# Kernel tuning notes

Hardware: AMD Instinct MI355X
Metric: run time of the kernel (lower is better)

## Reference

```python
import jax, jax.numpy as jnp
import numpy as np

V, B, F = 4, 8192, 128  # views, batch, fea_out
EPS = 1e-5  # torch BatchNorm1d default eps


def setup_inputs() -> dict:
    key = jax.random.key(0)
    k1, k2 = jax.random.split(key)
    x = jax.random.normal(k1, (V, B, F), dtype=jnp.float32)
    # Linear(F*F -> F) weight/bias; scale ~ kaiming-ish to keep activations sane
    W = jax.random.normal(k2, (F, F * F), dtype=jnp.float32) * 0.01
    b = jnp.zeros((F,), dtype=jnp.float32)
    gamma = jnp.ones((F,), dtype=jnp.float32)   # BN weight
    beta = jnp.zeros((F,), dtype=jnp.float32)   # BN bias
    return {"x": x, "W": W, "b": b, "gamma": gamma, "beta": beta}


def reference(x, W, b, gamma, beta):
    # x: [V, B, F] stack of views. Original loops over pairs (i<j):
    #   outer = x[i][:, :, None] @ x[j][:, None, :]          -> [B, F, F]
    #   flat  = outer.view(B, F*F)   (flat index = i*F + j)
    #   out   = ReLU(BN(Linear(flat)))
    # We fuse: Linear(flat(outer)) == einsum over W reshaped to [F_out, F, F],
    # avoiding the [B, F*F] intermediate. Same math.
    Vn, Bn, Fn = x.shape
    ii, jj = np.triu_indices(Vn, k=1)          # P = V*(V-1)/2 pairs
    x1 = x[ii]                                  # [P, B, F]
    x2 = x[jj]                                  # [P, B, F]
    Wr = W.reshape(Fn, Fn, Fn)                  # [F_out, F_i, F_j], matches row-major flatten
    # bilinear form per pair/batch: y[p,b,o] = sum_ij x1[p,b,i] * Wr[o,i,j] * x2[p,b,j] + b[o]
    y = jnp.einsum('pbi,oij,pbj->pbo', x1, Wr, x2) + b
    # BatchNorm1d in training mode: per-call batch stats (over batch axis, per pair),
    # biased variance, then affine, then ReLU.
    mean = jnp.mean(y, axis=1, keepdims=True)
    var = jnp.var(y, axis=1, keepdims=True)
    y_hat = (y - mean) * jax.lax.rsqrt(var + EPS)
    out = jax.nn.relu(gamma * y_hat + beta)     # [P, B, F]
    return out
```

## Files before the change

kernel.cpp:

```cpp
#include <hip/hip_runtime.h>

#define Fdim 128
#define Bsz  8192
#define Pn   6
#define EPSI 1e-5f
#define X2P 136
#define X1P 72

typedef _Float16 half8  __attribute__((ext_vector_type(8)));
typedef _Float16 half4t __attribute__((ext_vector_type(4)));
typedef float    float4t __attribute__((ext_vector_type(4)));

__constant__ int PAIR_A[6] = {0,0,0,1,1,2};
__constant__ int PAIR_B[6] = {1,2,3,2,3,3};

__global__ __launch_bounds__(256) void wprep(const float* __restrict__ W,
                                             _Float16* __restrict__ Wws) {
    int t    = blockIdx.x * 256 + threadIdx.x;
    int c    = t >> 9;
    int r    = t & 511;
    int nt   = r >> 6;
    int lane = r & 63;
    int q    = lane >> 4;
    int ol   = lane & 15;
    int o    = nt * 16 + ol;
    const float4t* src = (const float4t*)(W + (size_t)o * 16384 + c * 32 + q * 8);
    float4t a0 = src[0];
    float4t a1 = src[1];
    half8 h;
    h[0] = (_Float16)a0[0]; h[1] = (_Float16)a0[1];
    h[2] = (_Float16)a0[2]; h[3] = (_Float16)a0[3];
    h[4] = (_Float16)a1[0]; h[5] = (_Float16)a1[1];
    h[6] = (_Float16)a1[2]; h[7] = (_Float16)a1[3];
    *(half8*)(Wws + (size_t)t * 8) = h;
}

__global__ __launch_bounds__(256, 3) void gemm(const float* __restrict__ x,
                                               const _Float16* __restrict__ Wws,
                                               _Float16* __restrict__ yws,
                                               float* __restrict__ ssum,
                                               float* __restrict__ ssq) {
    __shared__ _Float16 x2t[128 * X2P];
    __shared__ _Float16 x1th[128 * X1P];

    int bid  = blockIdx.x;
    int p    = bid >> 7;
    int rem  = bid & 127;
    int mblk = rem >> 1;
    int nh   = rem & 1;
    int m0   = mblk * 128;
    int v1   = PAIR_A[p];
    int v2   = PAIR_B[p];
    int tid  = threadIdx.x;

    {
        const float4t* s2p = (const float4t*)(x + ((size_t)v2 * Bsz + m0) * Fdim);
        for (int it = 0; it < 16; ++it) {
            int idx = it * 256 + tid;
            int row = idx >> 5;
            int col = (idx & 31) * 4;
            float4t b = s2p[idx];
            half4t h2; h2[0]=(_Float16)b[0]; h2[1]=(_Float16)b[1];
                       h2[2]=(_Float16)b[2]; h2[3]=(_Float16)b[3];
            *(half4t*)&x2t[row * X2P + col] = h2;
        }
    }

    int lane  = tid & 63;
    int w     = tid >> 6;
    int wrow  = w >> 1;
    int wcol  = w & 1;
    int ol    = lane & 15;
    int q     = lane >> 4;
    int ntg0  = nh * 4 + wcol * 2;
    int ntg1  = ntg0 + 1;
    int rbase = wrow * 64;

    float4t acc[4][2];
#pragma unroll
    for (int mt = 0; mt < 4; ++mt) {
        acc[mt][0] = (float4t){0.f, 0.f, 0.f, 0.f};
        acc[mt][1] = (float4t){0.f, 0.f, 0.f, 0.f};
    }

    const half8* wb = (const half8*)Wws;
    const size_t woff0 = (size_t)ntg0 * 64 + lane;
    const size_t woff1 = (size_t)ntg1 * 64 + lane;
    const float* x1src = x + ((size_t)v1 * Bsz + m0) * Fdim;

    for (int kh = 0; kh < 2; ++kh) {
        if (kh) __syncthreads();
        for (int it = 0; it < 8; ++it) {
            int idx = it * 256 + tid;
            int row = idx >> 4;
            int c4  = (idx & 15) * 4;
            float4t a = *(const float4t*)(x1src + (size_t)row * Fdim + kh * 64 + c4);
            half4t h1; h1[0]=(_Float16)a[0]; h1[1]=(_Float16)a[1];
                       h1[2]=(_Float16)a[2]; h1[3]=(_Float16)a[3];
            *(half4t*)&x1th[row * X1P + c4] = h1;
        }
        __syncthreads();

        int ibase = kh * 64;
        for (int jc = 0; jc < 4; ++jc) {
            half8 x2f[4];
#pragma unroll
            for (int mt = 0; mt < 4; ++mt)
                x2f[mt] = *(const half8*)&x2t[(rbase + mt * 16 + ol) * X2P + jc * 32 + q * 8];

            half8 bfa0 = wb[(size_t)((ibase + 0) * 4 + jc) * 512 + woff0];
            half8 bfa1 = wb[(size_t)((ibase + 0) * 4 + jc) * 512 + woff1];
            half8 bfb0 = wb[(size_t)((ibase + 1) * 4 + jc) * 512 + woff0];
            half8 bfb1 = wb[(size_t)((ibase + 1) * 4 + jc) * 512 + woff1];

            for (int i8 = 0; i8 < 8; ++i8) {
                half8 x1f[4];
#pragma unroll
                for (int mt = 0; mt < 4; ++mt)
                    x1f[mt] = *(const half8*)&x1th[(rbase + mt * 16 + ol) * X1P + i8 * 8];
#pragma unroll
                for (int ii = 0; ii < 8; ++ii) {
                    int il  = i8 * 8 + ii;
                    int ipl = (il < 62) ? (il + 2) : 63;
                    half8 bn0 = wb[(size_t)((ibase + ipl) * 4 + jc) * 512 + woff0];
                    half8 bn1 = wb[(size_t)((ibase + ipl) * 4 + jc) * 512 + woff1];
#pragma unroll
                    for (int mt = 0; mt < 4; ++mt) {
                        _Float16 sc = x1f[mt][ii];
                        half8 a = x2f[mt] * sc;
                        acc[mt][0] = __builtin_amdgcn_mfma_f32_16x16x32_f16(a, bfa0, acc[mt][0], 0, 0, 0);
                        acc[mt][1] = __builtin_amdgcn_mfma_f32_16x16x32_f16(a, bfa1, acc[mt][1], 0, 0, 0);
                    }
                    bfa0 = bfb0; bfa1 = bfb1;
                    bfb0 = bn0;  bfb1 = bn1;
                }
            }
        }
    }

    float sum0 = 0.f, sq0 = 0.f, sum1 = 0.f, sq1 = 0.f;
    int col0 = ntg0 * 16 + ol;
    int col1 = ntg1 * 16 + ol;
#pragma unroll
    for (int mt = 0; mt < 4; ++mt) {
#pragma unroll
        for (int r = 0; r < 4; ++r) {
            size_t row = (size_t)p * Bsz + m0 + rbase + mt * 16 + q * 4 + r;
            float v0 = acc[mt][0][r];
            sum0 += v0; sq0 += v0 * v0;
            yws[row * Fdim + col0] = (_Float16)v0;
            float v1e = acc[mt][1][r];
            sum1 += v1e; sq1 += v1e * v1e;
            yws[row * Fdim + col1] = (_Float16)v1e;
        }
    }
    sum0 += __shfl_xor(sum0, 16, 64);  sum0 += __shfl_xor(sum0, 32, 64);
    sq0  += __shfl_xor(sq0, 16, 64);   sq0  += __shfl_xor(sq0, 32, 64);
    sum1 += __shfl_xor(sum1, 16, 64);  sum1 += __shfl_xor(sum1, 32, 64);
    sq1  += __shfl_xor(sq1, 16, 64);   sq1  += __shfl_xor(sq1, 32, 64);
    if (q == 0) {
        atomicAdd(&ssum[p * Fdim + col0], sum0);
        atomicAdd(&ssq [p * Fdim + col0], sq0);
        atomicAdd(&ssum[p * Fdim + col1], sum1);
        atomicAdd(&ssq [p * Fdim + col1], sq1);
    }
}

__global__ __launch_bounds__(256) void bnrelu(const _Float16* __restrict__ yws,
                                              const float* __restrict__ ssum,
                                              const float* __restrict__ ssq,
                                              const float* __restrict__ gamma,
                                              const float* __restrict__ beta,
                                              float* __restrict__ out) {
    __shared__ float gs[128], sh[128];
    size_t ebase = (size_t)blockIdx.x * 1024;
    int p = (int)(ebase >> 20);
    int t = threadIdx.x;
    if (t < 128) {
        float mean = ssum[p * Fdim + t] * (1.0f / 8192.0f);
        float var  = ssq [p * Fdim + t] * (1.0f / 8192.0f) - mean * mean;
        float g    = gamma[t] * rsqrtf(var + EPSI);
        gs[t] = g;
        sh[t] = beta[t] - g * mean;
    }
    __syncthreads();
    size_t e0 = ebase + (size_t)t * 4;
    int o0 = (int)(e0 & 127);
    half4t y = *(const half4t*)(yws + e0);
    float4t r;
#pragma unroll
    for (int l = 0; l < 4; ++l) {
        float v = fmaf(gs[o0 + l], (float)y[l], sh[o0 + l]);
        r[l] = v > 0.f ? v : 0.f;
    }
    *(float4t*)(out + e0) = r;
}

extern "C" void kernel_launch(void* const* d_in, const int* in_sizes, int n_in,
                              void* d_out, int out_size, void* d_ws, size_t ws_size,
                              hipStream_t stream) {
    const float* x     = (const float*)d_in[0];
    const float* W     = (const float*)d_in[1];
    const float* gamma = (const float*)d_in[3];
    const float* beta  = (const float*)d_in[4];
    float* out = (float*)d_out;

    char* ws = (char*)d_ws;
    _Float16* yws = (_Float16*)ws;
    _Float16* Wws = (_Float16*)(ws + 12582912);
    float*    ssum = (float*)(ws + 16777216);
    float*    ssq  = ssum + Pn * Fdim;

    (void)hipMemsetAsync(ssum, 0, 2 * Pn * Fdim * sizeof(float), stream);
    wprep<<<1024, 256, 0, stream>>>(W, Wws);
    gemm<<<768, 256, 0, stream>>>(x, Wws, yws, ssum, ssq);
    bnrelu<<<6144, 256, 0, stream>>>(yws, ssum, ssq, gamma, beta, out);
}
```

Measured before the change: 268.9 us.

## Split K across wave pairs so each wave computes four N tiles

Reassigns warps so the two waves in each row pair split the j-chunk (K) dimension instead of the output columns. Each wave now accumulates a 64x64 output tile (four N tiles) over half of K. The point is to reuse each scaled x2 A-fragment across four MFMAs instead of two, which halves the per-MFMA A-scaling work. In exchange, partial sums must be reduced through shared memory at the end, which adds barriers, and each wave holds twice as many accumulator registers. That extra register pressure may hurt occupancy under launch_bounds(256,3).

New measurement: 814.2 us. 203% more time.

```diff
diff --git a/kernel.cpp b/kernel.cpp
--- a/kernel.cpp
+++ b/kernel.cpp
@@ -40,8 +40,8 @@
                                                _Float16* __restrict__ yws,
                                                float* __restrict__ ssum,
                                                float* __restrict__ ssq) {
-    __shared__ _Float16 x2t[128 * X2P];
-    __shared__ _Float16 x1th[128 * X1P];
+    __shared__ __align__(16) _Float16 x2t[128 * X2P];
+    __shared__ __align__(16) _Float16 x1th[128 * X1P];
 
     int bid  = blockIdx.x;
     int p    = bid >> 7;
@@ -69,23 +69,20 @@
     int lane  = tid & 63;
     int w     = tid >> 6;
     int wrow  = w >> 1;
-    int wcol  = w & 1;
+    int kw    = w & 1;
     int ol    = lane & 15;
     int q     = lane >> 4;
-    int ntg0  = nh * 4 + wcol * 2;
-    int ntg1  = ntg0 + 1;
     int rbase = wrow * 64;
 
-    float4t acc[4][2];
-#pragma unroll
-    for (int mt = 0; mt < 4; ++mt) {
-        acc[mt][0] = (float4t){0.f, 0.f, 0.f, 0.f};
-        acc[mt][1] = (float4t){0.f, 0.f, 0.f, 0.f};
-    }
+    float4t acc[4][4];
+#pragma unroll
+    for (int mt = 0; mt < 4; ++mt)
+#pragma unroll
+        for (int nt = 0; nt < 4; ++nt)
+            acc[mt][nt] = (float4t){0.f, 0.f, 0.f, 0.f};
 
     const half8* wb = (const half8*)Wws;
-    const size_t woff0 = (size_t)ntg0 * 64 + lane;
-    const size_t woff1 = (size_t)ntg1 * 64 + lane;
+    const size_t wlane = (size_t)nh * 256 + lane;
     const float* x1src = x + ((size_t)v1 * Bsz + m0) * Fdim;
 
     for (int kh = 0; kh < 2; ++kh) {
@@ -101,68 +98,92 @@
         }
         __syncthreads();
 
-        int ibase = kh * 64;
-        for (int jc = 0; jc < 4; ++jc) {
+        for (int jcl = 0; jcl < 2; ++jcl) {
+            int jc = kw * 2 + jcl;
             half8 x2f[4];
 #pragma unroll
             for (int mt = 0; mt < 4; ++mt)
                 x2f[mt] = *(const half8*)&x2t[(rbase + mt * 16 + ol) * X2P + jc * 32 + q * 8];
 
-            half8 bfa0 = wb[(size_t)((ibase + 0) * 4 + jc) * 512 + woff0];
-            half8 bfa1 = wb[(size_t)((ibase + 0) * 4 + jc) * 512 + woff1];
-            half8 bfb0 = wb[(size_t)((ibase + 1) * 4 + jc) * 512 + woff0];
-            half8 bfb1 = wb[(size_t)((ibase + 1) * 4 + jc) * 512 + woff1];
-
-            for (int i8 = 0; i8 < 8; ++i8) {
+            size_t wbase = (size_t)(kh * 256 + jc) * 512 + wlane;
+            half8 bfa[4], bfb[4];
+#pragma unroll
+            for (int nt = 0; nt < 4; ++nt) bfa[nt] = wb[wbase + nt * 64];
+#pragma unroll
+            for (int nt = 0; nt < 4; ++nt) bfb[nt] = wb[wbase + 2048 + nt * 64];
+
+            for (int il8 = 0; il8 < 8; ++il8) {
                 half8 x1f[4];
 #pragma unroll
                 for (int mt = 0; mt < 4; ++mt)
-                    x1f[mt] = *(const half8*)&x1th[(rbase + mt * 16 + ol) * X1P + i8 * 8];
+                    x1f[mt] = *(const half8*)&x1th[(rbase + mt * 16 + ol) * X1P + il8 * 8];
 #pragma unroll
                 for (int ii = 0; ii < 8; ++ii) {
-                    int il  = i8 * 8 + ii;
+                    int il  = il8 * 8 + ii;
                     int ipl = (il < 62) ? (il + 2) : 63;
-                    half8 bn0 = wb[(size_t)((ibase + ipl) * 4 + jc) * 512 + woff0];
-                    half8 bn1 = wb[(size_t)((ibase + ipl) * 4 + jc) * 512 + woff1];
+                    half8 bn[4];
+#pragma unroll
+                    for (int nt = 0; nt < 4; ++nt)
+                        bn[nt] = wb[wbase + (size_t)ipl * 2048 + nt * 64];
 #pragma unroll
                     for (int mt = 0; mt < 4; ++mt) {
                         _Float16 sc = x1f[mt][ii];
                         half8 a = x2f[mt] * sc;
-                        acc[mt][0] = __builtin_amdgcn_mfma_f32_16x16x32_f16(a, bfa0, acc[mt][0], 0, 0, 0);
-                        acc[mt][1] = __builtin_amdgcn_mfma_f32_16x16x32_f16(a, bfa1, acc[mt][1], 0, 0, 0);
+#pragma unroll
+                        for (int nt = 0; nt < 4; ++nt)
+                            acc[mt][nt] = __builtin_amdgcn_mfma_f32_16x16x32_f16(a, bfa[nt], acc[mt][nt], 0, 0, 0);
                     }
-                    bfa0 = bfb0; bfa1 = bfb1;
-                    bfb0 = bn0;  bfb1 = bn1;
+#pragma unroll
+                    for (int nt = 0; nt < 4; ++nt) { bfa[nt] = bfb[nt]; bfb[nt] = bn[nt]; }
                 }
             }
         }
     }
 
-    float sum0 = 0.f, sq0 = 0.f, sum1 = 0.f, sq1 = 0.f;
-    int col0 = ntg0 * 16 + ol;
-    int col1 = ntg1 * 16 + ol;
-#pragma unroll
-    for (int mt = 0; mt < 4; ++mt) {
-#pragma unroll
-        for (int r = 0; r < 4; ++r) {
-            size_t row = (size_t)p * Bsz + m0 + rbase + mt * 16 + q * 4 + r;
-            float v0 = acc[mt][0][r];
-            sum0 += v0; sq0 += v0 * v0;
-            yws[row * Fdim + col0] = (_Float16)v0;
-            float v1e = acc[mt][1][r];
-            sum1 += v1e; sq1 += v1e * v1e;
-            yws[row * Fdim + col1] = (_Float16)v1e;
-        }
-    }
-    sum0 += __shfl_xor(sum0, 16, 64);  sum0 += __shfl_xor(sum0, 32, 64);
-    sq0  += __shfl_xor(sq0, 16, 64);   sq0  += __shfl_xor(sq0, 32, 64);
-    sum1 += __shfl_xor(sum1, 16, 64);  sum1 += __shfl_xor(sum1, 32, 64);
-    sq1  += __shfl_xor(sq1, 16, 64);   sq1  += __shfl_xor(sq1, 32, 64);
-    if (q == 0) {
-        atomicAdd(&ssum[p * Fdim + col0], sum0);
-        atomicAdd(&ssq [p * Fdim + col0], sq0);
-        atomicAdd(&ssum[p * Fdim + col1], sum1);
-        atomicAdd(&ssq [p * Fdim + col1], sq1);
+    __syncthreads();
+    float4t* xch = (float4t*)x2t;
+    if (kw == 1) {
+#pragma unroll
+        for (int mt = 0; mt < 4; ++mt)
+#pragma unroll
+            for (int nt = 0; nt < 4; ++nt)
+                xch[wrow * 1024 + (mt * 4 + nt) * 64 + lane] = acc[mt][nt];
+    }
+    __syncthreads();
+    if (kw == 0) {
+#pragma unroll
+        for (int mt = 0; mt < 4; ++mt)
+#pragma unroll
+            for (int nt = 0; nt < 4; ++nt)
+                acc[mt][nt] += xch[wrow * 1024 + (mt * 4 + nt) * 64 + lane];
+
+        float sum[4] = {0.f, 0.f, 0.f, 0.f};
+        float sq[4]  = {0.f, 0.f, 0.f, 0.f};
+#pragma unroll
+        for (int mt = 0; mt < 4; ++mt) {
+#pragma unroll
+            for (int r = 0; r < 4; ++r) {
+                size_t row = (size_t)p * Bsz + m0 + rbase + mt * 16 + q * 4 + r;
+#pragma unroll
+                for (int nt = 0; nt < 4; ++nt) {
+                    float v = acc[mt][nt][r];
+                    sum[nt] += v; sq[nt] += v * v;
+                    yws[row * Fdim + nh * 64 + nt * 16 + ol] = (_Float16)v;
+                }
+            }
+        }
+#pragma unroll
+        for (int nt = 0; nt < 4; ++nt) {
+            sum[nt] += __shfl_xor(sum[nt], 16, 64);  sum[nt] += __shfl_xor(sum[nt], 32, 64);
+            sq[nt]  += __shfl_xor(sq[nt], 16, 64);   sq[nt]  += __shfl_xor(sq[nt], 32, 64);
+        }
+        if (q == 0) {
+#pragma unroll
+            for (int nt = 0; nt < 4; ++nt) {
+                atomicAdd(&ssum[p * Fdim + nh * 64 + nt * 16 + ol], sum[nt]);
+                atomicAdd(&ssq [p * Fdim + nh * 64 + nt * 16 + ol], sq[nt]);
+            }
+        }
     }
 }
 
```

## Switch bilinear GEMM to 32x32x16 MFMA with relaid W and ring prefetch

Applied to the files above, without the earlier changes.

The main GEMM moves from 16x16x32 to 32x32x16 MFMA tiles. Each wave now covers a 64x32 output tile with two 16-wide accumulators, which halves the per-step scaling multiplies of the x2 fragments and the number of MFMA issues. W is preprocessed into a matching 32-column fragment layout and streamed through a four-deep register ring, with sched barriers added to steer the compiler's scheduling. LDS padding is reduced to 130 and 66 halves, which leaves 16-byte fragment reads on non-16-byte-aligned addresses and may cause split or slower LDS accesses.

Result: slower. 287.7 us (+7.0%).

```diff
diff --git a/kernel.cpp b/kernel.cpp
--- a/kernel.cpp
+++ b/kernel.cpp
@@ -4,12 +4,13 @@
 #define Bsz  8192
 #define Pn   6
 #define EPSI 1e-5f
-#define X2P 136
-#define X1P 72
-
-typedef _Float16 half8  __attribute__((ext_vector_type(8)));
-typedef _Float16 half4t __attribute__((ext_vector_type(4)));
+#define X2P 130
+#define X1P 66
+
+typedef _Float16 half8   __attribute__((ext_vector_type(8)));
+typedef _Float16 half4t  __attribute__((ext_vector_type(4)));
 typedef float    float4t __attribute__((ext_vector_type(4)));
+typedef float    float16t __attribute__((ext_vector_type(16)));
 
 __constant__ int PAIR_A[6] = {0,0,0,1,1,2};
 __constant__ int PAIR_B[6] = {1,2,3,2,3,3};
@@ -17,14 +18,16 @@
 __global__ __launch_bounds__(256) void wprep(const float* __restrict__ W,
                                              _Float16* __restrict__ Wws) {
     int t    = blockIdx.x * 256 + threadIdx.x;
-    int c    = t >> 9;
-    int r    = t & 511;
-    int nt   = r >> 6;
-    int lane = r & 63;
-    int q    = lane >> 4;
-    int ol   = lane & 15;
-    int o    = nt * 16 + ol;
-    const float4t* src = (const float4t*)(W + (size_t)o * 16384 + c * 32 + q * 8);
+    int f    = t >> 6;
+    int lane = t & 63;
+    int ntile = f >> 10;
+    int jc    = (f >> 7) & 7;
+    int i     = f & 127;
+    int q1 = lane >> 5;
+    int nn = lane & 31;
+    int n  = ntile * 32 + nn;
+    int k0 = i * 128 + jc * 16 + q1 * 8;
+    const float4t* src = (const float4t*)(W + (size_t)n * 16384 + k0);
     float4t a0 = src[0];
     float4t a1 = src[1];
     half8 h;
@@ -40,8 +43,8 @@
                                                _Float16* __restrict__ yws,
                                                float* __restrict__ ssum,
                                                float* __restrict__ ssq) {
-    __shared__ _Float16 x2t[128 * X2P];
-    __shared__ _Float16 x1th[128 * X1P];
+    __shared__ __align__(16) _Float16 x2t[128 * X2P];
+    __shared__ __align__(16) _Float16 x1th[128 * X1P];
 
     int bid  = blockIdx.x;
     int p    = bid >> 7;
@@ -70,22 +73,19 @@
     int w     = tid >> 6;
     int wrow  = w >> 1;
     int wcol  = w & 1;
-    int ol    = lane & 15;
-    int q     = lane >> 4;
-    int ntg0  = nh * 4 + wcol * 2;
-    int ntg1  = ntg0 + 1;
+    int nn    = lane & 31;
+    int q1    = lane >> 5;
+    int ntile = nh * 2 + wcol;
     int rbase = wrow * 64;
 
-    float4t acc[4][2];
-#pragma unroll
-    for (int mt = 0; mt < 4; ++mt) {
-        acc[mt][0] = (float4t){0.f, 0.f, 0.f, 0.f};
-        acc[mt][1] = (float4t){0.f, 0.f, 0.f, 0.f};
-    }
+    float16t acc[2];
+#pragma unroll
+    for (int mt = 0; mt < 2; ++mt)
+#pragma unroll
+        for (int e = 0; e < 16; ++e)
+            acc[mt][e] = 0.f;
 
     const half8* wb = (const half8*)Wws;
-    const size_t woff0 = (size_t)ntg0 * 64 + lane;
-    const size_t woff1 = (size_t)ntg1 * 64 + lane;
     const float* x1src = x + ((size_t)v1 * Bsz + m0) * Fdim;
 
     for (int kh = 0; kh < 2; ++kh) {
@@ -101,68 +101,56 @@
         }
         __syncthreads();
 
-        int ibase = kh * 64;
-        for (int jc = 0; jc < 4; ++jc) {
-            half8 x2f[4];
-#pragma unroll
-            for (int mt = 0; mt < 4; ++mt)
-                x2f[mt] = *(const half8*)&x2t[(rbase + mt * 16 + ol) * X2P + jc * 32 + q * 8];
-
-            half8 bfa0 = wb[(size_t)((ibase + 0) * 4 + jc) * 512 + woff0];
-            half8 bfa1 = wb[(size_t)((ibase + 0) * 4 + jc) * 512 + woff1];
-            half8 bfb0 = wb[(size_t)((ibase + 1) * 4 + jc) * 512 + woff0];
-            half8 bfb1 = wb[(size_t)((ibase + 1) * 4 + jc) * 512 + woff1];
-
-            for (int i8 = 0; i8 < 8; ++i8) {
-                half8 x1f[4];
-#pragma unroll
-                for (int mt = 0; mt < 4; ++mt)
-                    x1f[mt] = *(const half8*)&x1th[(rbase + mt * 16 + ol) * X1P + i8 * 8];
+#pragma unroll 1
+        for (int jc = 0; jc < 8; ++jc) {
+            half8 x2f[2];
+#pragma unroll
+            for (int mt = 0; mt < 2; ++mt)
+                x2f[mt] = *(const half8*)&x2t[(rbase + mt * 32 + nn) * X2P + jc * 16 + q1 * 8];
+
+            unsigned woff = (unsigned)((ntile * 1024 + jc * 128 + kh * 64) * 64 + lane);
+            half8 wbuf[4];
+#pragma unroll
+            for (int d = 0; d < 4; ++d) wbuf[d] = wb[woff + d * 64];
+
+#pragma unroll
+            for (int il8 = 0; il8 < 8; ++il8) {
+                half8 x1f[2];
+#pragma unroll
+                for (int mt = 0; mt < 2; ++mt)
+                    x1f[mt] = *(const half8*)&x1th[(rbase + mt * 32 + nn) * X1P + il8 * 8];
 #pragma unroll
                 for (int ii = 0; ii < 8; ++ii) {
-                    int il  = i8 * 8 + ii;
-                    int ipl = (il < 62) ? (il + 2) : 63;
-                    half8 bn0 = wb[(size_t)((ibase + ipl) * 4 + jc) * 512 + woff0];
-                    half8 bn1 = wb[(size_t)((ibase + ipl) * 4 + jc) * 512 + woff1];
-#pragma unroll
-                    for (int mt = 0; mt < 4; ++mt) {
-                        _Float16 sc = x1f[mt][ii];
-                        half8 a = x2f[mt] * sc;
-                        acc[mt][0] = __builtin_amdgcn_mfma_f32_16x16x32_f16(a, bfa0, acc[mt][0], 0, 0, 0);
-                        acc[mt][1] = __builtin_amdgcn_mfma_f32_16x16x32_f16(a, bfa1, acc[mt][1], 0, 0, 0);
-                    }
-                    bfa0 = bfb0; bfa1 = bfb1;
-                    bfb0 = bn0;  bfb1 = bn1;
+                    const int il = il8 * 8 + ii;
+                    half8 a0 = x2f[0] * x1f[0][ii];
+                    half8 a1 = x2f[1] * x1f[1][ii];
+                    acc[0] = __builtin_amdgcn_mfma_f32_32x32x16_f16(a0, wbuf[il & 3], acc[0], 0, 0, 0);
+                    acc[1] = __builtin_amdgcn_mfma_f32_32x32x16_f16(a1, wbuf[il & 3], acc[1], 0, 0, 0);
+                    wbuf[il & 3] = wb[woff + (unsigned)(il + 4) * 64];
                 }
+                __builtin_amdgcn_sched_barrier(0);
             }
         }
     }
 
-    float sum0 = 0.f, sq0 = 0.f, sum1 = 0.f, sq1 = 0.f;
-    int col0 = ntg0 * 16 + ol;
-    int col1 = ntg1 * 16 + ol;
-#pragma unroll
-    for (int mt = 0; mt < 4; ++mt) {
-#pragma unroll
-        for (int r = 0; r < 4; ++r) {
-            size_t row = (size_t)p * Bsz + m0 + rbase + mt * 16 + q * 4 + r;
-            float v0 = acc[mt][0][r];
-            sum0 += v0; sq0 += v0 * v0;
-            yws[row * Fdim + col0] = (_Float16)v0;
-            float v1e = acc[mt][1][r];
-            sum1 += v1e; sq1 += v1e * v1e;
-            yws[row * Fdim + col1] = (_Float16)v1e;
-        }
-    }
-    sum0 += __shfl_xor(sum0, 16, 64);  sum0 += __shfl_xor(sum0, 32, 64);
-    sq0  += __shfl_xor(sq0, 16, 64);   sq0  += __shfl_xor(sq0, 32, 64);
-    sum1 += __shfl_xor(sum1, 16, 64);  sum1 += __shfl_xor(sum1, 32, 64);
-    sq1  += __shfl_xor(sq1, 16, 64);   sq1  += __shfl_xor(sq1, 32, 64);
-    if (q == 0) {
-        atomicAdd(&ssum[p * Fdim + col0], sum0);
-        atomicAdd(&ssq [p * Fdim + col0], sq0);
-        atomicAdd(&ssum[p * Fdim + col1], sum1);
-        atomicAdd(&ssq [p * Fdim + col1], sq1);
+    float sum = 0.f, sq = 0.f;
+    int colg = ntile * 32 + nn;
+#pragma unroll
+    for (int mt = 0; mt < 2; ++mt) {
+#pragma unroll
+        for (int r = 0; r < 16; ++r) {
+            int rl = (r & 3) + 8 * (r >> 2) + 4 * q1;
+            size_t row = (size_t)p * Bsz + m0 + rbase + mt * 32 + rl;
+            float v = acc[mt][r];
+            sum += v; sq += v * v;
+            yws[row * Fdim + colg] = (_Float16)v;
+        }
+    }
+    sum += __shfl_xor(sum, 32, 64);
+    sq  += __shfl_xor(sq, 32, 64);
+    if (q1 == 0) {
+        atomicAdd(&ssum[p * Fdim + colg], sum);
+        atomicAdd(&ssq [p * Fdim + colg], sq);
     }
 }
 
@@ -206,8 +194,8 @@
     float* out = (float*)d_out;
 
     char* ws = (char*)d_ws;
-    _Float16* yws = (_Float16*)ws;
-    _Float16* Wws = (_Float16*)(ws + 12582912);
+    _Float16* Wws = (_Float16*)ws;
+    _Float16* yws = (_Float16*)(ws + 4194304);
     float*    ssum = (float*)(ws + 16777216);
     float*    ssq  = ssum + Pn * Fdim;
 
```
